# Performance work log

Measured on AMD Instinct MI355X. Metric: run time of the kernel, lower is better.

Reference implementation:

```python
import jax, jax.numpy as jnp
import numpy as np

B, D_IN, D_OUT, N_SUBNET, G = 16384, 512, 512, 8, 2


def setup_inputs() -> dict:
    key = jax.random.key(0)
    k_x, k_g, k_w = jax.random.split(key, 3)
    x = jax.random.normal(k_x, (B, D_IN), dtype=jnp.float32)
    groups = jax.random.randint(k_g, (B, G), 0, N_SUBNET, dtype=jnp.int32)
    # per-expert Dense params (the 'subnets')
    W = jax.random.normal(k_w, (N_SUBNET, D_IN, D_OUT), dtype=jnp.float32) * (1.0 / np.sqrt(D_IN))
    b = jnp.zeros((N_SUBNET, D_OUT), dtype=jnp.float32)
    return {"x": x, "groups": groups, "W": W, "b": b}


def reference(x, groups, W, b):
    """SubnetGate: one-hot gated dispatch to per-group subnets + combine.

    Faithful math: gates = one_hot(groups[:, group_col], n_subnet);
    out = sum_e gates[:, e] * subnet_e(x). Since gates are one-hot the
    combine selects exactly one expert output per row (gate weight 1.0).
    """
    group_col = 0
    n_subnet = W.shape[0]
    idx_group = groups[:, group_col]                     # [B]
    gates = jax.nn.one_hot(idx_group, n_subnet, dtype=x.dtype)  # [B, E]
    # run every expert on the full batch (dense reference for the
    # gather-compute-scatter kernel), then gate-combine
    expert_out = jnp.einsum("bi,eio->beo", x, W) + b[None, :, :]  # [B, E, O]
    out = jnp.einsum("be,beo->bo", gates, expert_out)             # [B, O]
    return out
```

## Files before the change

### kernel.cpp

```cpp
#include <hip/hip_runtime.h>
#include <hip/hip_bf16.h>


#define NROWS   16384
#define KDIM    512
#define NDIM    512
#define NEXP    8
#define BM      128
#define BN      128
#define BK      64
#define NT_PER  4
#define KT_PER  8
#define TILE_ELEMS (BN * BK)
#define WS_ROWLIST_OFF 4096
#define WS_WT_OFF      (4096 + NEXP * NROWS * 4)
#define WS_XG_OFF      (WS_WT_OFF + (size_t)NEXP * NT_PER * KT_PER * TILE_ELEMS * 2)
#define WS_NEEDED      (WS_XG_OFF + (size_t)NROWS * KDIM * 2)

typedef __bf16        bf16x8 __attribute__((ext_vector_type(8)));
typedef float         f32x4  __attribute__((ext_vector_type(4)));
typedef unsigned int  u32x4  __attribute__((ext_vector_type(4)));

__device__ __forceinline__ unsigned int f2bf_u(float f) {
    unsigned int u = __builtin_bit_cast(unsigned int, f);
    return (u + 0x7FFFu + ((u >> 16) & 1u)) >> 16;
}

__device__ __forceinline__ void gl_lds16(const void* g, void* l) {
    __builtin_amdgcn_global_load_lds(
        (const __attribute__((address_space(1))) unsigned int*)g,
        (__attribute__((address_space(3))) unsigned int*)l, 16, 0, 0);
}

__device__ __forceinline__ bf16x8 pack_bf8(f32x4 lo, f32x4 hi) {
    u32x4 w;
    w.x = f2bf_u(lo.x) | (f2bf_u(lo.y) << 16);
    w.y = f2bf_u(lo.z) | (f2bf_u(lo.w) << 16);
    w.z = f2bf_u(hi.x) | (f2bf_u(hi.y) << 16);
    w.w = f2bf_u(hi.z) | (f2bf_u(hi.w) << 16);
    return __builtin_bit_cast(bf16x8, w);
}

__global__ void prep_kernel(const float* __restrict__ W,
                            const float* __restrict__ x,
                            const int* __restrict__ groups,
                            int* __restrict__ counts,
                            int* __restrict__ rowlist,
                            unsigned short* __restrict__ Wtile,
                            unsigned short* __restrict__ xg) {
    const int bid = blockIdx.x;
    const int tid = threadIdx.x;

    if (bid < 8) {
        __shared__ int wcnt_s[4];
        __shared__ int woff_s[4];
        __shared__ int runb;
        const int e  = bid;
        const int w  = tid >> 6;
        const int ln = tid & 63;
        const unsigned long long below = (ln == 63) ? ~0ull >> 1
                                                    : (1ull << ln) - 1;
        int* dst = rowlist + e * NROWS;
        if (tid == 0) runb = 0;
        __syncthreads();
        for (int it = 0; it < NROWS / 1024; ++it) {
            int rbase = it * 1024 + tid * 4;
            u32x4 ga = *(const u32x4*)&groups[rbase * 2];
            u32x4 gb = *(const u32x4*)&groups[rbase * 2 + 4];
            bool h0 = ((int)ga.x == e), h1 = ((int)ga.z == e);
            bool h2 = ((int)gb.x == e), h3 = ((int)gb.z == e);
            unsigned long long m0 = __ballot(h0), m1 = __ballot(h1);
            unsigned long long m2 = __ballot(h2), m3 = __ballot(h3);
            int c0 = __popcll(m0), c1 = __popcll(m1), c2 = __popcll(m2);
            if (ln == 0) wcnt_s[w] = c0 + c1 + c2 + __popcll(m3);
            __syncthreads();
            if (tid == 0) {
                int s = runb;
                #pragma unroll
                for (int i = 0; i < 4; ++i) { woff_s[i] = s; s += wcnt_s[i]; }
                runb = s;
            }
            __syncthreads();
            int base = woff_s[w];
            if (h0) dst[base + __popcll(m0 & below)] = rbase;
            if (h1) dst[base + c0 + __popcll(m1 & below)] = rbase + 1;
            if (h2) dst[base + c0 + c1 + __popcll(m2 & below)] = rbase + 2;
            if (h3) dst[base + c0 + c1 + c2 + __popcll(m3 & below)] = rbase + 3;
            __syncthreads();
        }
        if (tid == 0) counts[e] = runb;
    } else if (bid < 1032) {
        __shared__ __align__(16) unsigned short tl4[32 * 64];
        const int tb   = bid - 8;
        const int tile = tb >> 2;
        const int qq   = tb & 3;
        const int e  = tile >> 5;
        const int nt = (tile >> 3) & 3;
        const int kt = tile & 7;
        const float* Wb = W + (size_t)e * (KDIM * NDIM);

        const int n   = qq * 32 + (tid & 31);
        const int g   = tid >> 5;
        const int col = nt * BN + n;
        unsigned int p[4];
        #pragma unroll
        for (int jj = 0; jj < 4; ++jj) {
            int k0 = kt * BK + g * 8 + jj * 2;
            unsigned int lo = f2bf_u(Wb[(size_t)k0 * NDIM + col]);
            unsigned int hi = f2bf_u(Wb[(size_t)(k0 + 1) * NDIM + col]);
            p[jj] = lo | (hi << 16);
        }
        *(u32x4*)&tl4[(n & 31) * 64 + (g ^ (n & 7)) * 8] = *(const u32x4*)p;
        __syncthreads();
        unsigned short* dst = Wtile + (size_t)tile * TILE_ELEMS
                                    + ((size_t)qq * 256 + tid) * 8;
        *(u32x4*)dst = *(const u32x4*)&tl4[tid * 8];
    } else {
        const size_t base = ((size_t)(bid - 1032) * 256 + tid) * 16;
        f32x4 v0 = *(const f32x4*)&x[base];
        f32x4 v1 = *(const f32x4*)&x[base + 4];
        f32x4 v2 = *(const f32x4*)&x[base + 8];
        f32x4 v3 = *(const f32x4*)&x[base + 12];
        *(bf16x8*)&xg[base]     = pack_bf8(v0, v1);
        *(bf16x8*)&xg[base + 8] = pack_bf8(v2, v3);
    }
}


#define STAGE_B(KT, BUF)                                                     \
    {                                                                        \
        const unsigned short* _src = wt + (size_t)(KT) * TILE_ELEMS;         \
        _Pragma("unroll")                                                    \
        for (int _i = 0; _i < 4; ++_i) {                                     \
            int _off = (_i * 256 + tid) * 8;                                 \
            gl_lds16(_src + _off, &Bsm[BUF][_off]);                          \
        }                                                                    \
    }

#define LOAD_A_XG(KT, AR)                                                    \
    {                                                                        \
        const unsigned short* _p0 = arow0 + (KT) * BK + q * 8;               \
        const unsigned short* _p1 = arow1 + (KT) * BK + q * 8;               \
        AR[0][0] = *(const bf16x8*)_p0;                                      \
        AR[0][1] = *(const bf16x8*)(_p0 + 32);                               \
        AR[1][0] = *(const bf16x8*)_p1;                                      \
        AR[1][1] = *(const bf16x8*)(_p1 + 32);                               \
    }

#define LOAD_A_F32(KT, AR)                                                   \
    {                                                                        \
        const float* _p0 = afrow0 + (KT) * BK + q * 8;                       \
        const float* _p1 = afrow1 + (KT) * BK + q * 8;                       \
        AR[0][0] = pack_bf8(*(const f32x4*)_p0, *(const f32x4*)(_p0 + 4));   \
        AR[0][1] = pack_bf8(*(const f32x4*)(_p0 + 32),                       \
                            *(const f32x4*)(_p0 + 36));                      \
        AR[1][0] = pack_bf8(*(const f32x4*)_p1, *(const f32x4*)(_p1 + 4));   \
        AR[1][1] = pack_bf8(*(const f32x4*)(_p1 + 32),                       \
                            *(const f32x4*)(_p1 + 36));                      \
    }

#define COMPUTE(BUF, AR)                                                     \
    {                                                                        \
        _Pragma("unroll")                                                    \
        for (int _h = 0; _h < 2; ++_h) {                                     \
            _Pragma("unroll")                                                \
            for (int _ni = 0; _ni < 8; ++_ni) {                              \
                int _n = _ni * 16 + l15;                                     \
                bf16x8 _bf = *(const bf16x8*)&Bsm[BUF][_n * 64 +             \
                             ((_h * 4 + q) ^ (_n & 7)) * 8];                 \
                acc[0][_ni] = __builtin_amdgcn_mfma_f32_16x16x32_bf16(       \
                    AR[0][_h], _bf, acc[0][_ni], 0, 0, 0);                   \
                acc[1][_ni] = __builtin_amdgcn_mfma_f32_16x16x32_bf16(       \
                    AR[1][_h], _bf, acc[1][_ni], 0, 0, 0);                   \
            }                                                                \
        }                                                                    \
    }

#define KSTEP(KT, ACUR, ANXT, LOADA)                                         \
    {                                                                        \
        asm volatile("s_waitcnt vmcnt(12)" ::: "memory");                    \
        __builtin_amdgcn_s_barrier();                                        \
        __builtin_amdgcn_sched_barrier(0);                                   \
        if ((KT) + 3 < KT_PER) STAGE_B((KT) + 3, ((KT) + 3) & 3)             \
        if ((KT) + 1 < KT_PER) LOADA((KT) + 1, ANXT)                         \
        __builtin_amdgcn_s_setprio(1);                                       \
        COMPUTE((KT) & 3, ACUR)                                              \
        __builtin_amdgcn_s_setprio(0);                                       \
    }

__global__ __launch_bounds__(256, 2)
void gemm_kernel(const float* __restrict__ x,
                 const unsigned short* __restrict__ xg,
                 const int* __restrict__ counts,
                 const int* __restrict__ rowlist,
                 const unsigned short* __restrict__ Wtile,
                 const float* __restrict__ bias,
                 float* __restrict__ out) {
    __shared__ __align__(16) unsigned short Bsm[4][TILE_ELEMS];

    const int bid = blockIdx.x;
    const int e   = bid & 7;
    const int j   = bid >> 3;
    const int nt  = j & 3;
    const int mt  = j >> 2;
    const int cnt = counts[e];
    const int rb  = mt * BM;
    if (rb >= cnt) return;
    int m_valid = cnt - rb;
    if (m_valid > BM) m_valid = BM;
    const int* rl = rowlist + e * NROWS + rb;

    const int tid = threadIdx.x;
    const int w   = tid >> 6;
    const int ln  = tid & 63;
    const int q   = ln >> 4;
    const int l15 = ln & 15;
    const int wm  = w * 32;

    const int r0i = wm + l15;
    const int r1i = wm + 16 + l15;
    const int ri0 = (r0i < m_valid) ? r0i : 0;
    const int ri1 = (r1i < m_valid) ? r1i : 0;

    const unsigned short* wt =
        Wtile + (size_t)((e * NT_PER + nt) * KT_PER) * TILE_ELEMS;

    f32x4 acc[2][8];
    #pragma unroll
    for (int mi = 0; mi < 2; ++mi)
        #pragma unroll
        for (int ni = 0; ni < 8; ++ni)
            acc[mi][ni] = (f32x4){0.f, 0.f, 0.f, 0.f};

    bf16x8 aA[2][2], aB[2][2];

    STAGE_B(0, 0)
    STAGE_B(1, 1)
    STAGE_B(2, 2)

    if (xg != nullptr) {
        const unsigned short* arow0 = xg + (size_t)rl[ri0] * KDIM;
        const unsigned short* arow1 = xg + (size_t)rl[ri1] * KDIM;
        LOAD_A_XG(0, aA)
        KSTEP(0, aA, aB, LOAD_A_XG)
        KSTEP(1, aB, aA, LOAD_A_XG)
        KSTEP(2, aA, aB, LOAD_A_XG)
        KSTEP(3, aB, aA, LOAD_A_XG)
        KSTEP(4, aA, aB, LOAD_A_XG)
        KSTEP(5, aB, aA, LOAD_A_XG)
        KSTEP(6, aA, aB, LOAD_A_XG)
        KSTEP(7, aB, aA, LOAD_A_XG)
    } else {
        const float* afrow0 = x + (size_t)rl[ri0] * KDIM;
        const float* afrow1 = x + (size_t)rl[ri1] * KDIM;
        LOAD_A_F32(0, aA)
        KSTEP(0, aA, aB, LOAD_A_F32)
        KSTEP(1, aB, aA, LOAD_A_F32)
        KSTEP(2, aA, aB, LOAD_A_F32)
        KSTEP(3, aB, aA, LOAD_A_F32)
        KSTEP(4, aA, aB, LOAD_A_F32)
        KSTEP(5, aB, aA, LOAD_A_F32)
        KSTEP(6, aA, aB, LOAD_A_F32)
        KSTEP(7, aB, aA, LOAD_A_F32)
    }

    int grow[2][4];
    #pragma unroll
    for (int mi = 0; mi < 2; ++mi)
        #pragma unroll
        for (int r = 0; r < 4; ++r) {
            int mloc = wm + mi * 16 + q * 4 + r;
            grow[mi][r] = (mloc < m_valid) ? rl[mloc] : -1;
        }
    const int ncol0 = nt * BN;
    #pragma unroll
    for (int ni = 0; ni < 8; ++ni) {
        int col = ncol0 + ni * 16 + l15;
        float bv = bias[e * NDIM + col];
        #pragma unroll
        for (int mi = 0; mi < 2; ++mi)
            #pragma unroll
            for (int r = 0; r < 4; ++r)
                if (grow[mi][r] >= 0)
                    __builtin_nontemporal_store(acc[mi][ni][r] + bv,
                        &out[(size_t)grow[mi][r] * NDIM + col]);
    }
}

extern "C" void kernel_launch(void* const* d_in, const int* in_sizes, int n_in,
                              void* d_out, int out_size, void* d_ws, size_t ws_size,
                              hipStream_t stream) {
    const float* x      = (const float*)d_in[0];
    const int*   groups = (const int*)d_in[1];
    const float* W      = (const float*)d_in[2];
    const float* b      = (const float*)d_in[3];
    float*       out    = (float*)d_out;

    char* ws = (char*)d_ws;
    int*            counts  = (int*)ws;
    int*            rowlist = (int*)(ws + WS_ROWLIST_OFF);
    unsigned short* Wtile   = (unsigned short*)(ws + WS_WT_OFF);
    const bool use_xg = (ws_size >= WS_NEEDED);
    unsigned short* xg = use_xg ? (unsigned short*)(ws + WS_XG_OFF) : nullptr;

    prep_kernel<<<use_xg ? 3080 : 1032, 256, 0, stream>>>(
        W, x, groups, counts, rowlist, Wtile, xg);
    gemm_kernel<<<4096, 256, 0, stream>>>(x, xg, counts, rowlist, Wtile, b, out);
}
```

Before: 132.4 us.

## Deepen A-operand register prefetch to two k-steps and widen rowlist scan

The GEMM main loop now triple-buffers the A fragments in registers (aA/aB/aC), issuing A loads two k-steps ahead instead of one, with per-step tuned vmcnt waits. The intent is to hide more global-load latency for the gathered rows. The rowlist builder also processes 8 rows per thread per iteration, halving the iterations and their barriers. The cost is more VGPRs under launch_bounds(256,2) and hand-computed waitcnt values that must match the exact order in which loads are issued.

```diff
diff --git a/kernel.cpp b/kernel.cpp
--- a/kernel.cpp
+++ b/kernel.cpp
@@ -63,16 +63,25 @@
         int* dst = rowlist + e * NROWS;
         if (tid == 0) runb = 0;
         __syncthreads();
-        for (int it = 0; it < NROWS / 1024; ++it) {
-            int rbase = it * 1024 + tid * 4;
-            u32x4 ga = *(const u32x4*)&groups[rbase * 2];
-            u32x4 gb = *(const u32x4*)&groups[rbase * 2 + 4];
-            bool h0 = ((int)ga.x == e), h1 = ((int)ga.z == e);
-            bool h2 = ((int)gb.x == e), h3 = ((int)gb.z == e);
-            unsigned long long m0 = __ballot(h0), m1 = __ballot(h1);
-            unsigned long long m2 = __ballot(h2), m3 = __ballot(h3);
-            int c0 = __popcll(m0), c1 = __popcll(m1), c2 = __popcll(m2);
-            if (ln == 0) wcnt_s[w] = c0 + c1 + c2 + __popcll(m3);
+        for (int it = 0; it < NROWS / 2048; ++it) {
+            int rbase = it * 2048 + tid * 8;
+            u32x4 g0 = *(const u32x4*)&groups[rbase * 2];
+            u32x4 g1 = *(const u32x4*)&groups[rbase * 2 + 4];
+            u32x4 g2 = *(const u32x4*)&groups[rbase * 2 + 8];
+            u32x4 g3 = *(const u32x4*)&groups[rbase * 2 + 12];
+            bool h[8] = {(int)g0.x == e, (int)g0.z == e,
+                         (int)g1.x == e, (int)g1.z == e,
+                         (int)g2.x == e, (int)g2.z == e,
+                         (int)g3.x == e, (int)g3.z == e};
+            unsigned long long m[8];
+            int c[8], tot = 0;
+            #pragma unroll
+            for (int jj = 0; jj < 8; ++jj) {
+                m[jj] = __ballot(h[jj]);
+                c[jj] = __popcll(m[jj]);
+                tot += c[jj];
+            }
+            if (ln == 0) wcnt_s[w] = tot;
             __syncthreads();
             if (tid == 0) {
                 int s = runb;
@@ -82,10 +91,11 @@
             }
             __syncthreads();
             int base = woff_s[w];
-            if (h0) dst[base + __popcll(m0 & below)] = rbase;
-            if (h1) dst[base + c0 + __popcll(m1 & below)] = rbase + 1;
-            if (h2) dst[base + c0 + c1 + __popcll(m2 & below)] = rbase + 2;
-            if (h3) dst[base + c0 + c1 + c2 + __popcll(m3 & below)] = rbase + 3;
+            #pragma unroll
+            for (int jj = 0; jj < 8; ++jj) {
+                if (h[jj]) dst[base + __popcll(m[jj] & below)] = rbase + jj;
+                base += c[jj];
+            }
             __syncthreads();
         }
         if (tid == 0) counts[e] = runb;
@@ -176,16 +186,30 @@
         }                                                                    \
     }
 
-#define KSTEP(KT, ACUR, ANXT, LOADA)                                         \
-    {                                                                        \
-        asm volatile("s_waitcnt vmcnt(12)" ::: "memory");                    \
+#define KSTEP(KT, VM, ACUR, ANXT, LOADA)                                     \
+    {                                                                        \
+        asm volatile("s_waitcnt vmcnt(" #VM ")" ::: "memory");               \
         __builtin_amdgcn_s_barrier();                                        \
         __builtin_amdgcn_sched_barrier(0);                                   \
+        if ((KT) + 2 < KT_PER) LOADA((KT) + 2, ANXT)                         \
         if ((KT) + 3 < KT_PER) STAGE_B((KT) + 3, ((KT) + 3) & 3)             \
-        if ((KT) + 1 < KT_PER) LOADA((KT) + 1, ANXT)                         \
         __builtin_amdgcn_s_setprio(1);                                       \
         COMPUTE((KT) & 3, ACUR)                                              \
         __builtin_amdgcn_s_setprio(0);                                       \
+    }
+
+#define KLOOP(LOADA)                                                         \
+    {                                                                        \
+        LOADA(0, aA)                                                         \
+        LOADA(1, aB)                                                         \
+        KSTEP(0, 16, aA, aC, LOADA)                                          \
+        KSTEP(1, 20, aB, aA, LOADA)                                          \
+        KSTEP(2, 24, aC, aB, LOADA)                                          \
+        KSTEP(3, 16, aA, aC, LOADA)                                          \
+        KSTEP(4, 16, aB, aA, LOADA)                                          \
+        KSTEP(5, 16, aC, aB, LOADA)                                          \
+        KSTEP(6, 12, aA, aC, LOADA)                                          \
+        KSTEP(7, 4,  aB, aA, LOADA)                                          \
     }
 
 __global__ __launch_bounds__(256, 2)
@@ -232,7 +256,7 @@
         for (int ni = 0; ni < 8; ++ni)
             acc[mi][ni] = (f32x4){0.f, 0.f, 0.f, 0.f};
 
-    bf16x8 aA[2][2], aB[2][2];
+    bf16x8 aA[2][2], aB[2][2], aC[2][2];
 
     STAGE_B(0, 0)
     STAGE_B(1, 1)
@@ -241,27 +265,11 @@
     if (xg != nullptr) {
         const unsigned short* arow0 = xg + (size_t)rl[ri0] * KDIM;
         const unsigned short* arow1 = xg + (size_t)rl[ri1] * KDIM;
-        LOAD_A_XG(0, aA)
-        KSTEP(0, aA, aB, LOAD_A_XG)
-        KSTEP(1, aB, aA, LOAD_A_XG)
-        KSTEP(2, aA, aB, LOAD_A_XG)
-        KSTEP(3, aB, aA, LOAD_A_XG)
-        KSTEP(4, aA, aB, LOAD_A_XG)
-        KSTEP(5, aB, aA, LOAD_A_XG)
-        KSTEP(6, aA, aB, LOAD_A_XG)
-        KSTEP(7, aB, aA, LOAD_A_XG)
+        KLOOP(LOAD_A_XG)
     } else {
         const float* afrow0 = x + (size_t)rl[ri0] * KDIM;
         const float* afrow1 = x + (size_t)rl[ri1] * KDIM;
-        LOAD_A_F32(0, aA)
-        KSTEP(0, aA, aB, LOAD_A_F32)
-        KSTEP(1, aB, aA, LOAD_A_F32)
-        KSTEP(2, aA, aB, LOAD_A_F32)
-        KSTEP(3, aB, aA, LOAD_A_F32)
-        KSTEP(4, aA, aB, LOAD_A_F32)
-        KSTEP(5, aB, aA, LOAD_A_F32)
-        KSTEP(6, aA, aB, LOAD_A_F32)
-        KSTEP(7, aB, aA, LOAD_A_F32)
+        KLOOP(LOAD_A_F32)
     }
 
     int grow[2][4];
```

Result: faster. 128.7 us (-2.8%).
